# Kernel tuning notes

Hardware: AMD Instinct MI355X
Metric: run time of the kernel (lower is better)

Reference implementation:

```python
import jax, jax.numpy as jnp
import numpy as np
import math

EMB = 768
B, S = 8, 2048

def setup_inputs() -> dict:
    key = jax.random.key(0)
    ks = jax.random.split(key, 6)
    q = jax.random.normal(ks[0], (B, S, EMB), dtype=jnp.float32)
    k = jax.random.normal(ks[1], (B, S, EMB), dtype=jnp.float32)
    v = jax.random.normal(ks[2], (B, S, EMB), dtype=jnp.float32)
    mask = jax.random.randint(ks[3], (B, S, S), 0, 2, dtype=jnp.int32)
    # nn.Linear(emb, emb): weight [out, in], bias [out]
    bound = 1.0 / math.sqrt(EMB)
    W = jax.random.uniform(ks[4], (EMB, EMB), minval=-bound, maxval=bound, dtype=jnp.float32)
    b = jax.random.uniform(ks[5], (EMB,), minval=-bound, maxval=bound, dtype=jnp.float32)
    return {"q": q, "k": k, "v": v, "mask": mask, "W": W, "b": b}

def reference(q, k, v, mask, W, b):
    # shared linear projection (torch Linear: x @ W^T + b)
    qp = jnp.einsum('bse,oe->bso', q, W) + b
    kp = jnp.einsum('bse,oe->bso', k, W) + b
    vp = jnp.einsum('bse,oe->bso', v, W) + b
    scores = jnp.einsum('bqe,bke->bqk', qp, kp) / math.sqrt(EMB)  # [B,S,S]
    scores = jnp.where(mask == 1, -jnp.inf, scores)
    attn = jax.nn.softmax(scores, axis=-1)
    return jnp.einsum('bqk,bke->bqe', attn, vp)
```

## Files before the change

kernel.cpp:

```cpp
#include <hip/hip_runtime.h>
#include <hip/hip_bf16.h>
#include <stdint.h>

#define B_ 8
#define S_ 2048
#define E_ 768

typedef __attribute__((ext_vector_type(4))) float f32x4;
typedef __attribute__((ext_vector_type(8))) short bf16x8;

#define A_TILE_USH (256 * 64)

__device__ __forceinline__ unsigned pk2bf(float x, float y) {
  unsigned r;
  asm("v_cvt_pk_bf16_f32 %0, %1, %2" : "=v"(r) : "v"(x), "v"(y));
  return r;
}

__device__ __forceinline__ void gll16(const void* g, void* l) {
  __builtin_amdgcn_global_load_lds((const __attribute__((address_space(1))) void*)g,
                                   (__attribute__((address_space(3))) void*)l, 16, 0, 0);
}

template <int BROWS>
__device__ __forceinline__ void stage_tile(const char* Ab, const char* Bb,
                                           int ldAb, int ldBb, int kt,
                                           unsigned short* As, unsigned short* Bs, int tid) {
#pragma unroll
  for (int i = 0; i < 4; ++i) {
    const unsigned lin = (unsigned)i * 8192u + (unsigned)tid * 16u;
    const unsigned row = lin >> 7, cb = lin & 127u;
    const unsigned cbs = cb ^ ((row & 7u) << 4);
    gll16(Ab + (size_t)row * ldAb + (size_t)kt * 128 + cbs, (char*)As + lin);
  }
#pragma unroll
  for (int i = 0; i < BROWS / 64; ++i) {
    const unsigned lin = (unsigned)i * 8192u + (unsigned)tid * 16u;
    const unsigned row = lin >> 7, cb = lin & 127u;
    const unsigned cbs = cb ^ ((row & 7u) << 4);
    gll16(Bb + (size_t)row * ldBb + (size_t)kt * 128 + cbs, (char*)Bs + lin);
  }
}

template <int NACC>
__device__ __forceinline__ void compute_tile(const unsigned short* As, const unsigned short* Bs,
                                             int wm, int wn, int lane, f32x4 (&acc)[4][NACC]) {
  bf16x8 af[4][2], bv[NACC][2];
#pragma unroll
  for (int m = 0; m < 4; ++m) {
    const int row = wm * 64 + m * 16 + (lane & 15);
#pragma unroll
    for (int ks = 0; ks < 2; ++ks) {
      const unsigned cb = ((unsigned)ks * 64u + (unsigned)(lane >> 4) * 16u) ^ (((unsigned)row & 7u) << 4);
      af[m][ks] = *reinterpret_cast<const bf16x8*>((const char*)As + row * 128 + cb);
    }
  }
#pragma unroll
  for (int n = 0; n < NACC; ++n) {
    const int row = wn * (NACC * 16) + n * 16 + (lane & 15);
#pragma unroll
    for (int ks = 0; ks < 2; ++ks) {
      const unsigned cb = ((unsigned)ks * 64u + (unsigned)(lane >> 4) * 16u) ^ (((unsigned)row & 7u) << 4);
      bv[n][ks] = *reinterpret_cast<const bf16x8*>((const char*)Bs + row * 128 + cb);
    }
  }
  __builtin_amdgcn_s_setprio(1);
#pragma unroll
  for (int ks = 0; ks < 2; ++ks)
#pragma unroll
    for (int m = 0; m < 4; ++m)
#pragma unroll
      for (int n = 0; n < NACC; ++n)
        acc[m][n] = __builtin_amdgcn_mfma_f32_16x16x32_bf16(af[m][ks], bv[n][ks], acc[m][n], 0, 0, 0);
  __builtin_amdgcn_s_setprio(0);
}

template <int BROWS, int NACC>
__device__ __forceinline__ void gemm_pipe(const char* Ab, const char* Bb, int ldAb, int ldBb,
                                          int NT, unsigned short* AsAll, unsigned short* BsAll,
                                          int tid, int wm, int wn, int lane,
                                          f32x4 (&acc)[4][NACC]) {
  constexpr int BT = BROWS * 64;
  constexpr int L = 4 + BROWS / 64;
  stage_tile<BROWS>(Ab, Bb, ldAb, ldBb, 0, AsAll, BsAll, tid);
  stage_tile<BROWS>(Ab, Bb, ldAb, ldBb, 1, AsAll + A_TILE_USH, BsAll + BT, tid);
  if constexpr (L == 6) asm volatile("s_waitcnt vmcnt(6)" ::: "memory");
  else                  asm volatile("s_waitcnt vmcnt(5)" ::: "memory");
  __builtin_amdgcn_s_barrier();
  __builtin_amdgcn_sched_barrier(0);
  for (int kt = 0; kt < NT; ++kt) {
    const int bk = kt % 3;
    if (kt + 2 < NT) {
      const int bs = (kt + 2) % 3;
      stage_tile<BROWS>(Ab, Bb, ldAb, ldBb, kt + 2, AsAll + bs * A_TILE_USH, BsAll + bs * BT, tid);
    }
    compute_tile<NACC>(AsAll + bk * A_TILE_USH, BsAll + bk * BT, wm, wn, lane, acc);
    if (kt + 1 < NT) {
      if (kt + 2 < NT) {
        if constexpr (L == 6) asm volatile("s_waitcnt vmcnt(6) lgkmcnt(0)" ::: "memory");
        else                  asm volatile("s_waitcnt vmcnt(5) lgkmcnt(0)" ::: "memory");
      } else {
        asm volatile("s_waitcnt vmcnt(0) lgkmcnt(0)" ::: "memory");
      }
      __builtin_amdgcn_s_barrier();
      __builtin_amdgcn_sched_barrier(0);
    }
  }
}

__global__ __launch_bounds__(256) void k_cvt(const float* __restrict__ q,
                                             const float* __restrict__ k,
                                             const float* __restrict__ v,
                                             const float* __restrict__ W,
                                             unsigned short* __restrict__ qb,
                                             unsigned short* __restrict__ kb,
                                             unsigned short* __restrict__ vb,
                                             unsigned short* __restrict__ Wb) {
  const int y = blockIdx.y;
  const float* src = (y == 0) ? q : (y == 1) ? k : (y == 2) ? v : W;
  unsigned short* dst = (y == 0) ? qb : (y == 1) ? kb : (y == 2) ? vb : Wb;
  const int n4 = (y < 3) ? (B_ * S_ * E_ / 4) : (E_ * E_ / 4);
  const int stride = gridDim.x * 256;
  for (int i = blockIdx.x * 256 + threadIdx.x; i < n4; i += stride) {
    float4 f = reinterpret_cast<const float4*>(src)[i];
    uint2 p;
    p.x = pk2bf(f.x, f.y);
    p.y = pk2bf(f.z, f.w);
    reinterpret_cast<uint2*>(dst)[i] = p;
  }
}

__global__ __launch_bounds__(512, 2) void k_projb(const unsigned short* __restrict__ Xb,
                                                  const unsigned short* __restrict__ Wb,
                                                  const float* __restrict__ bias,
                                                  unsigned short* __restrict__ qp,
                                                  unsigned short* __restrict__ kp,
                                                  unsigned short* __restrict__ vp) {
  __shared__ __attribute__((aligned(16))) unsigned short AsAll[3 * A_TILE_USH];
  __shared__ __attribute__((aligned(16))) unsigned short BsAll[3 * 128 * 64];
  const int tid = threadIdx.x, lane = tid & 63, wid = tid >> 6;
  const int wm = wid >> 1, wn = wid & 1;
  const int r0 = blockIdx.x * 256, c0 = blockIdx.y * 128, z = blockIdx.z;
  const unsigned short* X = Xb + (size_t)z * (B_ * S_ * E_);
  unsigned short* O = (z == 0) ? qp : ((z == 1) ? kp : vp);

  const char* Ab = (const char*)(X + (size_t)r0 * E_);
  const char* Bb = (const char*)(Wb + (size_t)c0 * E_);
  f32x4 acc[4][4] = {};
  gemm_pipe<128, 4>(Ab, Bb, E_ * 2, E_ * 2, E_ / 64, AsAll, BsAll, tid, wm, wn, lane, acc);

  float bcol[4];
#pragma unroll
  for (int n = 0; n < 4; ++n) bcol[n] = bias[c0 + wn * 64 + n * 16 + (lane & 15)];
#pragma unroll
  for (int m = 0; m < 4; ++m)
#pragma unroll
    for (int r = 0; r < 4; ++r) {
      const int row = r0 + wm * 64 + m * 16 + (lane >> 4) * 4 + r;
      const int colb = c0 + wn * 64 + (lane & 15);
      unsigned pkA = pk2bf(acc[m][0][r] + bcol[0], acc[m][1][r] + bcol[1]);
      unsigned pkB = pk2bf(acc[m][2][r] + bcol[2], acc[m][3][r] + bcol[3]);
      O[(size_t)row * E_ + colb]      = (unsigned short)pkA;
      O[(size_t)row * E_ + colb + 16] = (unsigned short)(pkA >> 16);
      O[(size_t)row * E_ + colb + 32] = (unsigned short)pkB;
      O[(size_t)row * E_ + colb + 48] = (unsigned short)(pkB >> 16);
    }
}

__global__ __launch_bounds__(256) void k_vtrans(const unsigned short* __restrict__ vp,
                                                unsigned short* __restrict__ vpT) {
  __shared__ __attribute__((aligned(16))) unsigned short t[64][72];
  const int tid = threadIdx.x;
  const int st = blockIdx.x;
  const int ot = blockIdx.y;
  const int b = blockIdx.z;
#pragma unroll
  for (int i = 0; i < 2; ++i) {
    int f = i * 256 + tid;
    int s = f >> 3, c8 = f & 7;
    uint4 vv = *reinterpret_cast<const uint4*>(
        &vp[((size_t)b * S_ + st * 64 + s) * E_ + ot * 64 + c8 * 8]);
    *reinterpret_cast<uint4*>(&t[s][c8 * 8]) = vv;
  }
  __syncthreads();
  const int o = tid >> 2;
  const int sb = (tid & 3) * 16;
  unsigned p[8];
#pragma unroll
  for (int j = 0; j < 8; ++j)
    p[j] = (unsigned)t[sb + 2 * j][o] | ((unsigned)t[sb + 2 * j + 1][o] << 16);
  uint4 w0 = make_uint4(p[0], p[1], p[2], p[3]);
  uint4 w1 = make_uint4(p[4], p[5], p[6], p[7]);
  size_t ob = ((size_t)b * E_ + ot * 64 + o) * S_ + st * 64 + sb;
  *reinterpret_cast<uint4*>(&vpT[ob]) = w0;
  *reinterpret_cast<uint4*>(&vpT[ob + 8]) = w1;
}

__global__ __launch_bounds__(512, 2) void k_scores(const unsigned short* __restrict__ qp,
                                                   const unsigned short* __restrict__ kp,
                                                   const int* __restrict__ mask,
                                                   unsigned short* __restrict__ P,
                                                   float* __restrict__ rowsum) {
  __shared__ __attribute__((aligned(16))) unsigned short AsAll[3 * A_TILE_USH];
  __shared__ __attribute__((aligned(16))) unsigned short BsAll[3 * 128 * 64];
  __shared__ float rlds[256][2];
  const int tid = threadIdx.x, lane = tid & 63, wid = tid >> 6;
  const int wm = wid >> 1, wn = wid & 1;
  const int qt = blockIdx.x, yt = blockIdx.y, b = blockIdx.z;
  const char* Ab = (const char*)(qp + ((size_t)b * S_ + qt * 256) * E_);
  const char* Bb = (const char*)(kp + ((size_t)b * S_ + yt * 128) * E_);
  f32x4 acc[4][4] = {};
  gemm_pipe<128, 4>(Ab, Bb, E_ * 2, E_ * 2, E_ / 64, AsAll, BsAll, tid, wm, wn, lane, acc);

  const float SC = (float)(1.4426950408889634 / 27.712812921102035);
  float rs[4][4];
#pragma unroll
  for (int m = 0; m < 4; ++m)
#pragma unroll
    for (int r = 0; r < 4; ++r) {
      const int grow = qt * 256 + wm * 64 + m * 16 + (lane >> 4) * 4 + r;
      const size_t rowoff = ((size_t)b * S_ + grow) * S_;
      const int cbase = yt * 128 + wn * 64 + (lane & 15);
      const int mk0 = mask[rowoff + cbase];
      const int mk1 = mask[rowoff + cbase + 16];
      const int mk2 = mask[rowoff + cbase + 32];
      const int mk3 = mask[rowoff + cbase + 48];
      float p0 = (mk0 == 1) ? 0.f : __builtin_amdgcn_exp2f(acc[m][0][r] * SC);
      float p1 = (mk1 == 1) ? 0.f : __builtin_amdgcn_exp2f(acc[m][1][r] * SC);
      float p2 = (mk2 == 1) ? 0.f : __builtin_amdgcn_exp2f(acc[m][2][r] * SC);
      float p3 = (mk3 == 1) ? 0.f : __builtin_amdgcn_exp2f(acc[m][3][r] * SC);
      unsigned pkA = pk2bf(p0, p1);
      unsigned pkB = pk2bf(p2, p3);
      P[rowoff + cbase]      = (unsigned short)pkA;
      P[rowoff + cbase + 16] = (unsigned short)(pkA >> 16);
      P[rowoff + cbase + 32] = (unsigned short)pkB;
      P[rowoff + cbase + 48] = (unsigned short)(pkB >> 16);
      rs[m][r] = (p0 + p1) + (p2 + p3);
    }

#pragma unroll
  for (int m = 0; m < 4; ++m)
#pragma unroll
    for (int r = 0; r < 4; ++r) {
      float vsum = rs[m][r];
      vsum += __shfl_xor(vsum, 1);
      vsum += __shfl_xor(vsum, 2);
      vsum += __shfl_xor(vsum, 4);
      vsum += __shfl_xor(vsum, 8);
      if ((lane & 15) == 0) rlds[wm * 64 + m * 16 + (lane >> 4) * 4 + r][wn] = vsum;
    }
  __syncthreads();
  if (tid < 256) {
    rowsum[(size_t)yt * (B_ * S_) + (size_t)b * S_ + qt * 256 + tid] =
        rlds[tid][0] + rlds[tid][1];
  }
}

__global__ __launch_bounds__(256) void k_invrs(const float* __restrict__ rowsum,
                                               float* __restrict__ inv_rs) {
  int i = blockIdx.x * 256 + threadIdx.x;
  float t = 0.f;
#pragma unroll
  for (int g = 0; g < 16; ++g) t += rowsum[(size_t)g * (B_ * S_) + i];
  inv_rs[i] = 1.0f / t;
}

__global__ __launch_bounds__(512, 2) void k_pv(const unsigned short* __restrict__ P,
                                               const unsigned short* __restrict__ vpT,
                                               const float* __restrict__ inv_rs,
                                               float* __restrict__ out) {
  __shared__ __attribute__((aligned(16))) unsigned short AsAll[3 * A_TILE_USH];
  __shared__ __attribute__((aligned(16))) unsigned short BsAll[3 * 64 * 64];
  const int tid = threadIdx.x, lane = tid & 63, wid = tid >> 6;
  const int wm = wid >> 1, wn = wid & 1;
  const int mt = blockIdx.x, yt = blockIdx.y, b = blockIdx.z;
  const char* Ab = (const char*)(P + ((size_t)b * S_ + mt * 256) * S_);
  const char* Bb = (const char*)(vpT + ((size_t)b * E_ + yt * 64) * S_);
  f32x4 acc[4][2] = {};
  gemm_pipe<64, 2>(Ab, Bb, S_ * 2, S_ * 2, S_ / 64, AsAll, BsAll, tid, wm, wn, lane, acc);

#pragma unroll
  for (int m = 0; m < 4; ++m)
#pragma unroll
    for (int r = 0; r < 4; ++r) {
      const int grow = mt * 256 + wm * 64 + m * 16 + (lane >> 4) * 4 + r;
      const float inv = inv_rs[b * S_ + grow];
      const int gcol = yt * 64 + wn * 32 + (lane & 15);
      out[((size_t)b * S_ + grow) * E_ + gcol]      = acc[m][0][r] * inv;
      out[((size_t)b * S_ + grow) * E_ + gcol + 16] = acc[m][1][r] * inv;
    }
}

extern "C" void kernel_launch(void* const* d_in, const int* in_sizes, int n_in,
                              void* d_out, int out_size, void* d_ws, size_t ws_size,
                              hipStream_t stream) {
  const float* q = (const float*)d_in[0];
  const float* k = (const float*)d_in[1];
  const float* v = (const float*)d_in[2];
  const int* mask = (const int*)d_in[3];
  const float* W = (const float*)d_in[4];
  const float* bias = (const float*)d_in[5];
  float* out = (float*)d_out;
  char* ws = (char*)d_ws;

  unsigned short* qb = (unsigned short*)(ws + 0);
  unsigned short* kb = (unsigned short*)(ws + 25165824);
  unsigned short* vb = (unsigned short*)(ws + 50331648);
  unsigned short* Wb = (unsigned short*)(ws + 75497472);
  unsigned short* qp = (unsigned short*)(ws + 76677120);
  unsigned short* kp = (unsigned short*)(ws + 101842944);
  unsigned short* vpT = (unsigned short*)(ws + 127008768);
  unsigned short* P = (unsigned short*)(ws + 0);
  float* rowsum = (float*)(ws + 75497472);
  float* inv_rs = (float*)(ws + 76546048);
  unsigned short* vp_tmp = (unsigned short*)d_out;
  (void)in_sizes; (void)n_in; (void)out_size; (void)ws_size;

  dim3 blk(256, 1, 1);
  dim3 blk2(512, 1, 1);
  k_cvt<<<dim3(512, 4, 1), blk, 0, stream>>>(q, k, v, W, qb, kb, vb, Wb);
  k_projb<<<dim3(64, 6, 3), blk2, 0, stream>>>(qb, Wb, bias, qp, kp, vp_tmp);
  k_vtrans<<<dim3(32, 12, 8), blk, 0, stream>>>(vp_tmp, vpT);
  k_scores<<<dim3(8, 16, 8), blk2, 0, stream>>>(qp, kp, mask, P, rowsum);
  k_invrs<<<dim3(64, 1, 1), blk, 0, stream>>>(rowsum, inv_rs);
  k_pv<<<dim3(8, 12, 8), blk2, 0, stream>>>(P, vpT, inv_rs, out);
}
```

Before: 337.5 us.

## Switch GEMMs to 256x256 tiles with K=32 four-stage pipeline

Replaces the shared GEMM pipeline with a 256x256 output tile per block: 8 waves in a 2x4 layout, each holding 8x4 accumulators. The K step shrinks to 32 with a new XOR swizzle, and the pipeline grows to four LDS stages with three loads in flight. All three GEMM kernels (projection, scores, PV) use it, and grid orders and the rowsum partition count are adjusted to match. The aim is higher arithmetic intensity and fewer global reloads per output. The cost is doubled accumulator registers (risking occupancy at launch bounds 512,2), fewer blocks per kernel, and narrower scalar stores in the epilogues.

```diff
diff --git a/kernel.cpp b/kernel.cpp
--- a/kernel.cpp
+++ b/kernel.cpp
@@ -9,7 +9,7 @@
 typedef __attribute__((ext_vector_type(4))) float f32x4;
 typedef __attribute__((ext_vector_type(8))) short bf16x8;
 
-#define A_TILE_USH (256 * 64)
+#define TILE_USH (256 * 32)
 
 __device__ __forceinline__ unsigned pk2bf(float x, float y) {
   unsigned r;
@@ -22,86 +22,73 @@
                                    (__attribute__((address_space(3))) void*)l, 16, 0, 0);
 }
 
-template <int BROWS>
-__device__ __forceinline__ void stage_tile(const char* Ab, const char* Bb,
-                                           int ldAb, int ldBb, int kt,
-                                           unsigned short* As, unsigned short* Bs, int tid) {
-#pragma unroll
-  for (int i = 0; i < 4; ++i) {
+__device__ __forceinline__ void stage32(const char* Ab, const char* Bb, int ldA, int ldB,
+                                        int kt, unsigned short* As, unsigned short* Bs,
+                                        int tid) {
+#pragma unroll
+  for (int i = 0; i < 2; ++i) {
     const unsigned lin = (unsigned)i * 8192u + (unsigned)tid * 16u;
-    const unsigned row = lin >> 7, cb = lin & 127u;
-    const unsigned cbs = cb ^ ((row & 7u) << 4);
-    gll16(Ab + (size_t)row * ldAb + (size_t)kt * 128 + cbs, (char*)As + lin);
-  }
-#pragma unroll
-  for (int i = 0; i < BROWS / 64; ++i) {
+    const unsigned row = lin >> 6;
+    const unsigned chunk = (lin >> 4) & 3u;
+    const unsigned sw = (chunk ^ ((row >> 1) & 3u)) << 4;
+    gll16(Ab + (size_t)row * ldA + (size_t)kt * 64 + sw, (char*)As + lin);
+  }
+#pragma unroll
+  for (int i = 0; i < 2; ++i) {
     const unsigned lin = (unsigned)i * 8192u + (unsigned)tid * 16u;
-    const unsigned row = lin >> 7, cb = lin & 127u;
-    const unsigned cbs = cb ^ ((row & 7u) << 4);
-    gll16(Bb + (size_t)row * ldBb + (size_t)kt * 128 + cbs, (char*)Bs + lin);
-  }
-}
-
-template <int NACC>
-__device__ __forceinline__ void compute_tile(const unsigned short* As, const unsigned short* Bs,
-                                             int wm, int wn, int lane, f32x4 (&acc)[4][NACC]) {
-  bf16x8 af[4][2], bv[NACC][2];
-#pragma unroll
-  for (int m = 0; m < 4; ++m) {
-    const int row = wm * 64 + m * 16 + (lane & 15);
-#pragma unroll
-    for (int ks = 0; ks < 2; ++ks) {
-      const unsigned cb = ((unsigned)ks * 64u + (unsigned)(lane >> 4) * 16u) ^ (((unsigned)row & 7u) << 4);
-      af[m][ks] = *reinterpret_cast<const bf16x8*>((const char*)As + row * 128 + cb);
-    }
-  }
-#pragma unroll
-  for (int n = 0; n < NACC; ++n) {
-    const int row = wn * (NACC * 16) + n * 16 + (lane & 15);
-#pragma unroll
-    for (int ks = 0; ks < 2; ++ks) {
-      const unsigned cb = ((unsigned)ks * 64u + (unsigned)(lane >> 4) * 16u) ^ (((unsigned)row & 7u) << 4);
-      bv[n][ks] = *reinterpret_cast<const bf16x8*>((const char*)Bs + row * 128 + cb);
-    }
+    const unsigned row = lin >> 6;
+    const unsigned chunk = (lin >> 4) & 3u;
+    const unsigned sw = (chunk ^ ((row >> 1) & 3u)) << 4;
+    gll16(Bb + (size_t)row * ldB + (size_t)kt * 64 + sw, (char*)Bs + lin);
+  }
+}
+
+__device__ __forceinline__ void compute32(const unsigned short* As, const unsigned short* Bs,
+                                          int wm, int wn, int lane, f32x4 (&acc)[8][4]) {
+  bf16x8 af[8], bf[4];
+  const unsigned ksw = (unsigned)(lane >> 4);
+#pragma unroll
+  for (int m = 0; m < 8; ++m) {
+    const unsigned row = (unsigned)(wm * 128 + m * 16 + (lane & 15));
+    const unsigned off = row * 64 + ((ksw ^ ((row >> 1) & 3u)) << 4);
+    af[m] = *reinterpret_cast<const bf16x8*>((const char*)As + off);
+  }
+#pragma unroll
+  for (int n = 0; n < 4; ++n) {
+    const unsigned row = (unsigned)(wn * 64 + n * 16 + (lane & 15));
+    const unsigned off = row * 64 + ((ksw ^ ((row >> 1) & 3u)) << 4);
+    bf[n] = *reinterpret_cast<const bf16x8*>((const char*)Bs + off);
   }
   __builtin_amdgcn_s_setprio(1);
 #pragma unroll
-  for (int ks = 0; ks < 2; ++ks)
-#pragma unroll
-    for (int m = 0; m < 4; ++m)
-#pragma unroll
-      for (int n = 0; n < NACC; ++n)
-        acc[m][n] = __builtin_amdgcn_mfma_f32_16x16x32_bf16(af[m][ks], bv[n][ks], acc[m][n], 0, 0, 0);
+  for (int m = 0; m < 8; ++m)
+#pragma unroll
+    for (int n = 0; n < 4; ++n)
+      acc[m][n] = __builtin_amdgcn_mfma_f32_16x16x32_bf16(af[m], bf[n], acc[m][n], 0, 0, 0);
   __builtin_amdgcn_s_setprio(0);
 }
 
-template <int BROWS, int NACC>
-__device__ __forceinline__ void gemm_pipe(const char* Ab, const char* Bb, int ldAb, int ldBb,
-                                          int NT, unsigned short* AsAll, unsigned short* BsAll,
-                                          int tid, int wm, int wn, int lane,
-                                          f32x4 (&acc)[4][NACC]) {
-  constexpr int BT = BROWS * 64;
-  constexpr int L = 4 + BROWS / 64;
-  stage_tile<BROWS>(Ab, Bb, ldAb, ldBb, 0, AsAll, BsAll, tid);
-  stage_tile<BROWS>(Ab, Bb, ldAb, ldBb, 1, AsAll + A_TILE_USH, BsAll + BT, tid);
-  if constexpr (L == 6) asm volatile("s_waitcnt vmcnt(6)" ::: "memory");
-  else                  asm volatile("s_waitcnt vmcnt(5)" ::: "memory");
+__device__ __forceinline__ void gemm_pipe32(const char* Ab, const char* Bb, int ldA, int ldB,
+                                            int NT, unsigned short* AsAll, unsigned short* BsAll,
+                                            int tid, int wm, int wn, int lane,
+                                            f32x4 (&acc)[8][4]) {
+  stage32(Ab, Bb, ldA, ldB, 0, AsAll, BsAll, tid);
+  stage32(Ab, Bb, ldA, ldB, 1, AsAll + TILE_USH, BsAll + TILE_USH, tid);
+  stage32(Ab, Bb, ldA, ldB, 2, AsAll + 2 * TILE_USH, BsAll + 2 * TILE_USH, tid);
+  asm volatile("s_waitcnt vmcnt(8)" ::: "memory");
   __builtin_amdgcn_s_barrier();
   __builtin_amdgcn_sched_barrier(0);
   for (int kt = 0; kt < NT; ++kt) {
-    const int bk = kt % 3;
-    if (kt + 2 < NT) {
-      const int bs = (kt + 2) % 3;
-      stage_tile<BROWS>(Ab, Bb, ldAb, ldBb, kt + 2, AsAll + bs * A_TILE_USH, BsAll + bs * BT, tid);
-    }
-    compute_tile<NACC>(AsAll + bk * A_TILE_USH, BsAll + bk * BT, wm, wn, lane, acc);
+    if (kt + 3 < NT) {
+      const int bs = (kt + 3) & 3;
+      stage32(Ab, Bb, ldA, ldB, kt + 3, AsAll + bs * TILE_USH, BsAll + bs * TILE_USH, tid);
+    }
+    const int bk = kt & 3;
+    compute32(AsAll + bk * TILE_USH, BsAll + bk * TILE_USH, wm, wn, lane, acc);
     if (kt + 1 < NT) {
-      if (kt + 2 < NT) {
-        if constexpr (L == 6) asm volatile("s_waitcnt vmcnt(6) lgkmcnt(0)" ::: "memory");
-        else                  asm volatile("s_waitcnt vmcnt(5) lgkmcnt(0)" ::: "memory");
-      } else {
-        asm volatile("s_waitcnt vmcnt(0) lgkmcnt(0)" ::: "memory");
-      }
+      if (kt + 3 < NT)       asm volatile("s_waitcnt vmcnt(8) lgkmcnt(0)" ::: "memory");
+      else if (kt + 3 == NT) asm volatile("s_waitcnt vmcnt(4) lgkmcnt(0)" ::: "memory");
+      else                   asm volatile("s_waitcnt vmcnt(0) lgkmcnt(0)" ::: "memory");
       __builtin_amdgcn_s_barrier();
       __builtin_amdgcn_sched_barrier(0);
     }
@@ -136,34 +123,32 @@
                                                   unsigned short* __restrict__ qp,
                                                   unsigned short* __restrict__ kp,
                                                   unsigned short* __restrict__ vp) {
-  __shared__ __attribute__((aligned(16))) unsigned short AsAll[3 * A_TILE_USH];
-  __shared__ __attribute__((aligned(16))) unsigned short BsAll[3 * 128 * 64];
+  __shared__ __attribute__((aligned(16))) unsigned short AsAll[4 * TILE_USH];
+  __shared__ __attribute__((aligned(16))) unsigned short BsAll[4 * TILE_USH];
   const int tid = threadIdx.x, lane = tid & 63, wid = tid >> 6;
-  const int wm = wid >> 1, wn = wid & 1;
-  const int r0 = blockIdx.x * 256, c0 = blockIdx.y * 128, z = blockIdx.z;
+  const int wm = wid >> 2, wn = wid & 3;
+  const int c0 = blockIdx.x * 256, r0 = blockIdx.y * 256, z = blockIdx.z;
   const unsigned short* X = Xb + (size_t)z * (B_ * S_ * E_);
   unsigned short* O = (z == 0) ? qp : ((z == 1) ? kp : vp);
 
   const char* Ab = (const char*)(X + (size_t)r0 * E_);
   const char* Bb = (const char*)(Wb + (size_t)c0 * E_);
-  f32x4 acc[4][4] = {};
-  gemm_pipe<128, 4>(Ab, Bb, E_ * 2, E_ * 2, E_ / 64, AsAll, BsAll, tid, wm, wn, lane, acc);
+  f32x4 acc[8][4] = {};
+  gemm_pipe32(Ab, Bb, E_ * 2, E_ * 2, E_ / 32, AsAll, BsAll, tid, wm, wn, lane, acc);
 
   float bcol[4];
 #pragma unroll
   for (int n = 0; n < 4; ++n) bcol[n] = bias[c0 + wn * 64 + n * 16 + (lane & 15)];
 #pragma unroll
-  for (int m = 0; m < 4; ++m)
+  for (int m = 0; m < 8; ++m)
 #pragma unroll
     for (int r = 0; r < 4; ++r) {
-      const int row = r0 + wm * 64 + m * 16 + (lane >> 4) * 4 + r;
-      const int colb = c0 + wn * 64 + (lane & 15);
-      unsigned pkA = pk2bf(acc[m][0][r] + bcol[0], acc[m][1][r] + bcol[1]);
-      unsigned pkB = pk2bf(acc[m][2][r] + bcol[2], acc[m][3][r] + bcol[3]);
-      O[(size_t)row * E_ + colb]      = (unsigned short)pkA;
-      O[(size_t)row * E_ + colb + 16] = (unsigned short)(pkA >> 16);
-      O[(size_t)row * E_ + colb + 32] = (unsigned short)pkB;
-      O[(size_t)row * E_ + colb + 48] = (unsigned short)(pkB >> 16);
+      const int row = r0 + wm * 128 + m * 16 + (lane >> 4) * 4 + r;
+#pragma unroll
+      for (int n = 0; n < 4; ++n) {
+        const int col = c0 + wn * 64 + n * 16 + (lane & 15);
+        O[(size_t)row * E_ + col] = (unsigned short)pk2bf(acc[m][n][r] + bcol[n], 0.f);
+      }
     }
 }
 
@@ -201,58 +186,46 @@
                                                    const int* __restrict__ mask,
                                                    unsigned short* __restrict__ P,
                                                    float* __restrict__ rowsum) {
-  __shared__ __attribute__((aligned(16))) unsigned short AsAll[3 * A_TILE_USH];
-  __shared__ __attribute__((aligned(16))) unsigned short BsAll[3 * 128 * 64];
-  __shared__ float rlds[256][2];
+  __shared__ __attribute__((aligned(16))) unsigned short AsAll[4 * TILE_USH];
+  __shared__ __attribute__((aligned(16))) unsigned short BsAll[4 * TILE_USH];
+  __shared__ float rlds[256][4];
   const int tid = threadIdx.x, lane = tid & 63, wid = tid >> 6;
-  const int wm = wid >> 1, wn = wid & 1;
-  const int qt = blockIdx.x, yt = blockIdx.y, b = blockIdx.z;
+  const int wm = wid >> 2, wn = wid & 3;
+  const int yt = blockIdx.x, qt = blockIdx.y, b = blockIdx.z;
   const char* Ab = (const char*)(qp + ((size_t)b * S_ + qt * 256) * E_);
-  const char* Bb = (const char*)(kp + ((size_t)b * S_ + yt * 128) * E_);
-  f32x4 acc[4][4] = {};
-  gemm_pipe<128, 4>(Ab, Bb, E_ * 2, E_ * 2, E_ / 64, AsAll, BsAll, tid, wm, wn, lane, acc);
+  const char* Bb = (const char*)(kp + ((size_t)b * S_ + yt * 256) * E_);
+  f32x4 acc[8][4] = {};
+  gemm_pipe32(Ab, Bb, E_ * 2, E_ * 2, E_ / 32, AsAll, BsAll, tid, wm, wn, lane, acc);
 
   const float SC = (float)(1.4426950408889634 / 27.712812921102035);
-  float rs[4][4];
-#pragma unroll
-  for (int m = 0; m < 4; ++m)
+#pragma unroll
+  for (int m = 0; m < 8; ++m)
 #pragma unroll
     for (int r = 0; r < 4; ++r) {
-      const int grow = qt * 256 + wm * 64 + m * 16 + (lane >> 4) * 4 + r;
+      const int rloc = wm * 128 + m * 16 + (lane >> 4) * 4 + r;
+      const int grow = qt * 256 + rloc;
       const size_t rowoff = ((size_t)b * S_ + grow) * S_;
-      const int cbase = yt * 128 + wn * 64 + (lane & 15);
-      const int mk0 = mask[rowoff + cbase];
-      const int mk1 = mask[rowoff + cbase + 16];
-      const int mk2 = mask[rowoff + cbase + 32];
-      const int mk3 = mask[rowoff + cbase + 48];
-      float p0 = (mk0 == 1) ? 0.f : __builtin_amdgcn_exp2f(acc[m][0][r] * SC);
-      float p1 = (mk1 == 1) ? 0.f : __builtin_amdgcn_exp2f(acc[m][1][r] * SC);
-      float p2 = (mk2 == 1) ? 0.f : __builtin_amdgcn_exp2f(acc[m][2][r] * SC);
-      float p3 = (mk3 == 1) ? 0.f : __builtin_amdgcn_exp2f(acc[m][3][r] * SC);
-      unsigned pkA = pk2bf(p0, p1);
-      unsigned pkB = pk2bf(p2, p3);
-      P[rowoff + cbase]      = (unsigned short)pkA;
-      P[rowoff + cbase + 16] = (unsigned short)(pkA >> 16);
-      P[rowoff + cbase + 32] = (unsigned short)pkB;
-      P[rowoff + cbase + 48] = (unsigned short)(pkB >> 16);
-      rs[m][r] = (p0 + p1) + (p2 + p3);
-    }
-
-#pragma unroll
-  for (int m = 0; m < 4; ++m)
-#pragma unroll
-    for (int r = 0; r < 4; ++r) {
-      float vsum = rs[m][r];
+      const int cbase = yt * 256 + wn * 64 + (lane & 15);
+      float radd = 0.f;
+#pragma unroll
+      for (int n = 0; n < 4; ++n) {
+        const int col = cbase + n * 16;
+        const int mk = mask[rowoff + col];
+        float pv = (mk == 1) ? 0.f : __builtin_amdgcn_exp2f(acc[m][n][r] * SC);
+        radd += pv;
+        P[rowoff + col] = (unsigned short)pk2bf(pv, 0.f);
+      }
+      float vsum = radd;
       vsum += __shfl_xor(vsum, 1);
       vsum += __shfl_xor(vsum, 2);
       vsum += __shfl_xor(vsum, 4);
       vsum += __shfl_xor(vsum, 8);
-      if ((lane & 15) == 0) rlds[wm * 64 + m * 16 + (lane >> 4) * 4 + r][wn] = vsum;
+      if ((lane & 15) == 0) rlds[rloc][wn] = vsum;
     }
   __syncthreads();
   if (tid < 256) {
     rowsum[(size_t)yt * (B_ * S_) + (size_t)b * S_ + qt * 256 + tid] =
-        rlds[tid][0] + rlds[tid][1];
+        (rlds[tid][0] + rlds[tid][1]) + (rlds[tid][2] + rlds[tid][3]);
   }
 }
 
@@ -261,7 +234,7 @@
   int i = blockIdx.x * 256 + threadIdx.x;
   float t = 0.f;
 #pragma unroll
-  for (int g = 0; g < 16; ++g) t += rowsum[(size_t)g * (B_ * S_) + i];
+  for (int g = 0; g < 8; ++g) t += rowsum[(size_t)g * (B_ * S_) + i];
   inv_rs[i] = 1.0f / t;
 }
 
@@ -269,25 +242,27 @@
                                                const unsigned short* __restrict__ vpT,
                                                const float* __restrict__ inv_rs,
                                                float* __restrict__ out) {
-  __shared__ __attribute__((aligned(16))) unsigned short AsAll[3 * A_TILE_USH];
-  __shared__ __attribute__((aligned(16))) unsigned short BsAll[3 * 64 * 64];
+  __shared__ __attribute__((aligned(16))) unsigned short AsAll[4 * TILE_USH];
+  __shared__ __attribute__((aligned(16))) unsigned short BsAll[4 * TILE_USH];
   const int tid = threadIdx.x, lane = tid & 63, wid = tid >> 6;
-  const int wm = wid >> 1, wn = wid & 1;
-  const int mt = blockIdx.x, yt = blockIdx.y, b = blockIdx.z;
+  const int wm = wid >> 2, wn = wid & 3;
+  const int yt = blockIdx.x, mt = blockIdx.y, b = blockIdx.z;
   const char* Ab = (const char*)(P + ((size_t)b * S_ + mt * 256) * S_);
-  const char* Bb = (const char*)(vpT + ((size_t)b * E_ + yt * 64) * S_);
-  f32x4 acc[4][2] = {};
-  gemm_pipe<64, 2>(Ab, Bb, S_ * 2, S_ * 2, S_ / 64, AsAll, BsAll, tid, wm, wn, lane, acc);
-
-#pragma unroll
-  for (int m = 0; m < 4; ++m)
+  const char* Bb = (const char*)(vpT + ((size_t)b * E_ + yt * 256) * S_);
+  f32x4 acc[8][4] = {};
+  gemm_pipe32(Ab, Bb, S_ * 2, S_ * 2, S_ / 32, AsAll, BsAll, tid, wm, wn, lane, acc);
+
+#pragma unroll
+  for (int m = 0; m < 8; ++m)
 #pragma unroll
     for (int r = 0; r < 4; ++r) {
-      const int grow = mt * 256 + wm * 64 + m * 16 + (lane >> 4) * 4 + r;
+      const int grow = mt * 256 + wm * 128 + m * 16 + (lane >> 4) * 4 + r;
       const float inv = inv_rs[b * S_ + grow];
-      const int gcol = yt * 64 + wn * 32 + (lane & 15);
-      out[((size_t)b * S_ + grow) * E_ + gcol]      = acc[m][0][r] * inv;
-      out[((size_t)b * S_ + grow) * E_ + gcol + 16] = acc[m][1][r] * inv;
+#pragma unroll
+      for (int n = 0; n < 4; ++n) {
+        const int col = yt * 256 + wn * 64 + n * 16 + (lane & 15);
+        out[((size_t)b * S_ + grow) * E_ + col] = acc[m][n][r] * inv;
+      }
     }
 }
 
@@ -319,9 +294,9 @@
   dim3 blk(256, 1, 1);
   dim3 blk2(512, 1, 1);
   k_cvt<<<dim3(512, 4, 1), blk, 0, stream>>>(q, k, v, W, qb, kb, vb, Wb);
-  k_projb<<<dim3(64, 6, 3), blk2, 0, stream>>>(qb, Wb, bias, qp, kp, vp_tmp);
+  k_projb<<<dim3(3, 64, 3), blk2, 0, stream>>>(qb, Wb, bias, qp, kp, vp_tmp);
   k_vtrans<<<dim3(32, 12, 8), blk, 0, stream>>>(vp_tmp, vpT);
-  k_scores<<<dim3(8, 16, 8), blk2, 0, stream>>>(qp, kp, mask, P, rowsum);
+  k_scores<<<dim3(8, 8, 8), blk2, 0, stream>>>(qp, kp, mask, P, rowsum);
   k_invrs<<<dim3(64, 1, 1), blk, 0, stream>>>(rowsum, inv_rs);
-  k_pv<<<dim3(8, 12, 8), blk2, 0, stream>>>(P, vpT, inv_rs, out);
-}
+  k_pv<<<dim3(3, 8, 8), blk2, 0, stream>>>(P, vpT, inv_rs, out);
+}
```

After: 359.3 us. 6.5% more time.
